# Performance work log

Measured on AMD Instinct MI355X. Metric: run time of the kernel, lower is better.

## Reference

```python
import jax, jax.numpy as jnp
import numpy as np

WINDOW_SIZE = 7
CHANNELS = 3
C1 = 0.01 ** 2
C2 = 0.03 ** 2


def _gaussian_window():
    # 1D gaussian, sigma=1.5, normalized; outer product -> 2D window
    coords = jnp.arange(WINDOW_SIZE, dtype=jnp.float32) - WINDOW_SIZE // 2
    g = jnp.exp(-coords ** 2 / (2 * 1.5 ** 2))
    g = g / g.sum()
    w2d = g[:, None] * g[None, :]  # [7,7]
    # depthwise kernel [C,1,7,7] (OIHW with feature_group_count=C)
    return jnp.tile(w2d[None, None], (CHANNELS, 1, 1, 1))


def _dwconv(x, window):
    pad = WINDOW_SIZE // 2
    return jax.lax.conv_general_dilated(
        x, window,
        window_strides=(1, 1),
        padding=[(pad, pad), (pad, pad)],
        dimension_numbers=('NCHW', 'OIHW', 'NCHW'),
        feature_group_count=CHANNELS,
    )


def setup_inputs() -> dict:
    key = jax.random.key(0)
    k1, k2 = jax.random.split(key)
    shape = (16, 3, 512, 512)
    enhanced = jax.random.uniform(k1, shape, dtype=jnp.float32)
    target = jax.random.uniform(k2, shape, dtype=jnp.float32)
    return {"enhanced": enhanced, "target": target}


def reference(enhanced, target):
    window = _gaussian_window()
    mu1 = _dwconv(enhanced, window)
    mu2 = _dwconv(target, window)
    mu1_sq = mu1 ** 2
    mu2_sq = mu2 ** 2
    mu1_mu2 = mu1 * mu2
    sigma1_sq = _dwconv(enhanced ** 2, window) - mu1_sq
    sigma2_sq = _dwconv(target ** 2, window) - mu2_sq
    sigma12 = _dwconv(enhanced * target, window) - mu1_mu2
    ssim_map = ((2 * mu1_mu2 + C1) * (2 * sigma12 + C2)) / (
        (mu1_sq + mu2_sq + C1) * (sigma1_sq + sigma2_sq + C2))
    return 1.0 - ssim_map.mean()
```

## Files before the change

kernel.cpp:

```cpp
#include <hip/hip_runtime.h>


#define TILE_W 64
#define TILE_H 16
#define HALO 3
#define IN_H 22
#define H_PAIRS 67
#define IMG_H 512
#define IMG_W 512
#define NPLANES 48
#define SSIM_C1 1.0e-4f
#define SSIM_C2 9.0e-4f

static __device__ constexpr float G[7] = {
    0.03663284536f, 0.11128076166f, 0.21674531251f, 0.27068216094f,
    0.21674531251f, 0.11128076166f, 0.03663284536f};

__device__ __forceinline__ float2 pk_fma(const float2 a, const float2 b,
                                         const float2 c) {
  float2 d;
  asm("v_pk_fma_f32 %0, %1, %2, %3" : "=v"(d) : "v"(a), "v"(b), "v"(c));
  return d;
}

__device__ __forceinline__ float4 ld4z(const float* __restrict__ row, int col) {
  if (col >= 0 && col + 3 < IMG_W) {
    return *reinterpret_cast<const float4*>(row + col);
  }
  float4 v;
  v.x = ((unsigned)(col + 0) < IMG_W) ? row[col + 0] : 0.f;
  v.y = ((unsigned)(col + 1) < IMG_W) ? row[col + 1] : 0.f;
  v.z = ((unsigned)(col + 2) < IMG_W) ? row[col + 2] : 0.f;
  v.w = ((unsigned)(col + 3) < IMG_W) ? row[col + 3] : 0.f;
  return v;
}

__global__ __launch_bounds__(256, 6) void ssim_tile_kernel(
    const float* __restrict__ x, const float* __restrict__ y,
    float* __restrict__ partial) {
  __shared__ __align__(16) float2 hbuf[2][IN_H][H_PAIRS];

  const int tid = threadIdx.x;
  const int plane = blockIdx.z;
  const float* __restrict__ xp = x + (size_t)plane * (IMG_H * IMG_W);
  const float* __restrict__ yp = y + (size_t)plane * (IMG_H * IMG_W);
  const int y0 = blockIdx.y * TILE_H - HALO;
  const int x0 = blockIdx.x * TILE_W;
  const bool edge = (blockIdx.x == 0) | (blockIdx.x == gridDim.x - 1) |
                    (blockIdx.y == 0) | (blockIdx.y == gridDim.y - 1);

  if (tid < IN_H * 8) {
    const int hr = tid >> 3;
    const int cg = tid & 7;
    const int bcol = x0 + 8 * cg - 4;
    float wx[16], wy[16];
    const int gy = y0 + hr;
    if (!edge) {
      const float* xr = xp + (size_t)gy * IMG_W + bcol;
      const float* yr = yp + (size_t)gy * IMG_W + bcol;
#pragma unroll
      for (int v = 0; v < 4; ++v) {
        const float4 a = *reinterpret_cast<const float4*>(xr + 4 * v);
        const float4 b = *reinterpret_cast<const float4*>(yr + 4 * v);
        wx[4 * v + 0] = a.x; wx[4 * v + 1] = a.y;
        wx[4 * v + 2] = a.z; wx[4 * v + 3] = a.w;
        wy[4 * v + 0] = b.x; wy[4 * v + 1] = b.y;
        wy[4 * v + 2] = b.z; wy[4 * v + 3] = b.w;
      }
    } else if ((unsigned)gy < IMG_H) {
      const float* xr = xp + (size_t)gy * IMG_W;
      const float* yr = yp + (size_t)gy * IMG_W;
#pragma unroll
      for (int v = 0; v < 4; ++v) {
        const float4 a = ld4z(xr, bcol + 4 * v);
        const float4 b = ld4z(yr, bcol + 4 * v);
        wx[4 * v + 0] = a.x; wx[4 * v + 1] = a.y;
        wx[4 * v + 2] = a.z; wx[4 * v + 3] = a.w;
        wy[4 * v + 0] = b.x; wy[4 * v + 1] = b.y;
        wy[4 * v + 2] = b.z; wy[4 * v + 3] = b.w;
      }
    } else {
#pragma unroll
      for (int i = 0; i < 16; ++i) { wx[i] = 0.f; wy[i] = 0.f; }
    }
    float2 A[8], B[8];
#pragma unroll
    for (int j = 0; j < 8; ++j) {
      A[j] = make_float2(0.f, 0.f);
      B[j] = make_float2(0.f, 0.f);
    }
#pragma unroll
    for (int wi = 1; wi < 15; ++wi) {
      const float xv = wx[wi];
      const float yv = wy[wi];
      const float2 xyp = make_float2(xv, yv);
      const float2 spp = make_float2(fmaf(xv, xv, yv * yv), xv * yv);
#pragma unroll
      for (int j = 0; j < 8; ++j) {
        const int k = wi - 1 - j;
        if (k >= 0 && k < 7) {
          const float2 gk2 = make_float2(G[k], G[k]);
          A[j] = pk_fma(gk2, xyp, A[j]);
          B[j] = pk_fma(gk2, spp, B[j]);
        }
      }
    }
    float2* b0 = &hbuf[0][hr][8 * cg];
    float2* b1 = &hbuf[1][hr][8 * cg];
#pragma unroll
    for (int j = 0; j < 8; ++j) {
      b0[j] = A[j];
      b1[j] = B[j];
    }
  }
  __syncthreads();

  const int c = tid & 63;
  const int r0 = (tid >> 6) * 4;
  float2 M[4], S4[4];
#pragma unroll
  for (int t = 0; t < 4; ++t) {
    M[t] = make_float2(0.f, 0.f);
    S4[t] = make_float2(0.f, 0.f);
  }
#pragma unroll
  for (int j = 0; j < 10; ++j) {
    const float2 mv = hbuf[0][r0 + j][c];
    const float2 sv = hbuf[1][r0 + j][c];
#pragma unroll
    for (int t = 0; t < 4; ++t) {
      const int k = j - t;
      if (k >= 0 && k < 7) {
        const float2 gk2 = make_float2(G[k], G[k]);
        M[t] = pk_fma(gk2, mv, M[t]);
        S4[t] = pk_fma(gk2, sv, S4[t]);
      }
    }
  }

  float acc = 0.f;
#pragma unroll
  for (int t = 0; t < 4; ++t) {
    const float mu1 = M[t].x, mu2 = M[t].y;
    const float eS = S4[t].x, eXY = S4[t].y;
    const float mu12 = mu1 * mu2;
    const float msq = fmaf(mu1, mu1, mu2 * mu2);
    const float sig12 = eXY - mu12;
    const float sigsum = eS - msq;
    const float num = fmaf(2.f, mu12, SSIM_C1) * fmaf(2.f, sig12, SSIM_C2);
    const float den = (msq + SSIM_C1) * (sigsum + SSIM_C2);
    float r = __builtin_amdgcn_rcpf(den);
    r = r * fmaf(-den, r, 2.f);
    acc = fmaf(num, r, acc);
  }

#pragma unroll
  for (int off = 32; off > 0; off >>= 1) acc += __shfl_down(acc, off, 64);
  __shared__ float wsum[4];
  if ((tid & 63) == 0) wsum[tid >> 6] = acc;
  __syncthreads();
  if (tid == 0) {
    const float s = wsum[0] + wsum[1] + wsum[2] + wsum[3];
    partial[(size_t)blockIdx.z * gridDim.x * gridDim.y +
            (size_t)blockIdx.y * gridDim.x + blockIdx.x] = s;
  }
}

__global__ __launch_bounds__(1024) void ssim_reduce_kernel(
    const float* __restrict__ partial, int n, float* __restrict__ out) {
  float acc = 0.f;
  const int nv = n >> 2;
  const float4* __restrict__ p4 = reinterpret_cast<const float4*>(partial);
  for (int i = threadIdx.x; i < nv; i += 1024) {
    const float4 v = p4[i];
    acc += (v.x + v.y) + (v.z + v.w);
  }
#pragma unroll
  for (int off = 32; off > 0; off >>= 1) acc += __shfl_down(acc, off, 64);
  __shared__ float wsum[16];
  if ((threadIdx.x & 63) == 0) wsum[threadIdx.x >> 6] = acc;
  __syncthreads();
  if (threadIdx.x == 0) {
    float s = 0.f;
#pragma unroll
    for (int w = 0; w < 16; ++w) s += wsum[w];
    out[0] = 1.f - s * (1.f / (float)(NPLANES * IMG_H * IMG_W));
  }
}

extern "C" void kernel_launch(void* const* d_in, const int* in_sizes, int n_in,
                              void* d_out, int out_size, void* d_ws, size_t ws_size,
                              hipStream_t stream) {
  const float* enhanced = (const float*)d_in[0];
  const float* target = (const float*)d_in[1];
  float* out = (float*)d_out;
  float* partial = (float*)d_ws;

  dim3 grid(IMG_W / TILE_W, IMG_H / TILE_H, NPLANES);
  dim3 block(256, 1, 1);
  ssim_tile_kernel<<<grid, block, 0, stream>>>(enhanced, target, partial);

  const int nblocks = (IMG_W / TILE_W) * (IMG_H / TILE_H) * NPLANES;
  ssim_reduce_kernel<<<1, 1024, 0, stream>>>(partial, nblocks, out);
}
```

Before: 158.2 us.

## Make each block sweep a full tile row with double-buffered LDS and prefetch

Each block now handles a whole 16-row strip of a plane, looping over the 8 column tiles instead of launching one block per tile. The next tile's global loads are issued before the current tile's vertical pass, and two LDS buffers alternate so that only one barrier per tile is needed. LDS writes are widened to float4, and the row padding changes from 67 to 66 to allow that. The aim is to hide global load latency and cut per-block launch and reduction overhead, at the cost of far fewer blocks (1536), lower occupancy (launch bounds 3) and possible LDS bank conflicts from the new padding.

```diff
diff --git a/kernel.cpp b/kernel.cpp
--- a/kernel.cpp
+++ b/kernel.cpp
@@ -5,10 +5,11 @@
 #define TILE_H 16
 #define HALO 3
 #define IN_H 22
-#define H_PAIRS 67
+#define H_PAIRS 66
 #define IMG_H 512
 #define IMG_W 512
 #define NPLANES 48
+#define NTX 8
 #define SSIM_C1 1.0e-4f
 #define SSIM_C2 9.0e-4f
 
@@ -35,54 +36,68 @@
   return v;
 }
 
-__global__ __launch_bounds__(256, 6) void ssim_tile_kernel(
+__device__ __forceinline__ void lds_barrier() {
+  __builtin_amdgcn_sched_barrier(0);
+  asm volatile("s_waitcnt lgkmcnt(0)" ::: "memory");
+  __builtin_amdgcn_s_barrier();
+  __builtin_amdgcn_sched_barrier(0);
+}
+
+__global__ __launch_bounds__(256, 3) void ssim_row_kernel(
     const float* __restrict__ x, const float* __restrict__ y,
     float* __restrict__ partial) {
-  __shared__ __align__(16) float2 hbuf[2][IN_H][H_PAIRS];
+  __shared__ __align__(16) float2 hbuf[2][2][IN_H][H_PAIRS];
 
   const int tid = threadIdx.x;
-  const int plane = blockIdx.z;
+  const int ty = blockIdx.x;
+  const int plane = blockIdx.y;
   const float* __restrict__ xp = x + (size_t)plane * (IMG_H * IMG_W);
   const float* __restrict__ yp = y + (size_t)plane * (IMG_H * IMG_W);
-  const int y0 = blockIdx.y * TILE_H - HALO;
-  const int x0 = blockIdx.x * TILE_W;
-  const bool edge = (blockIdx.x == 0) | (blockIdx.x == gridDim.x - 1) |
-                    (blockIdx.y == 0) | (blockIdx.y == gridDim.y - 1);
-
-  if (tid < IN_H * 8) {
-    const int hr = tid >> 3;
-    const int cg = tid & 7;
-    const int bcol = x0 + 8 * cg - 4;
-    float wx[16], wy[16];
-    const int gy = y0 + hr;
+  const int y0 = ty * TILE_H - HALO;
+  const bool edge_y = (ty == 0) | (ty == 31);
+
+  const int hr = tid >> 3;
+  const int cg = tid & 7;
+  const bool active = tid < IN_H * 8;
+  const int gy = y0 + hr;
+
+  float4 px[4], py[4];
+
+  auto load_tile = [&](int tx) {
+    const int bcol = tx * TILE_W + 8 * cg - 4;
+    const bool edge = edge_y | (tx == 0) | (tx == NTX - 1);
     if (!edge) {
       const float* xr = xp + (size_t)gy * IMG_W + bcol;
       const float* yr = yp + (size_t)gy * IMG_W + bcol;
 #pragma unroll
       for (int v = 0; v < 4; ++v) {
-        const float4 a = *reinterpret_cast<const float4*>(xr + 4 * v);
-        const float4 b = *reinterpret_cast<const float4*>(yr + 4 * v);
-        wx[4 * v + 0] = a.x; wx[4 * v + 1] = a.y;
-        wx[4 * v + 2] = a.z; wx[4 * v + 3] = a.w;
-        wy[4 * v + 0] = b.x; wy[4 * v + 1] = b.y;
-        wy[4 * v + 2] = b.z; wy[4 * v + 3] = b.w;
+        px[v] = *reinterpret_cast<const float4*>(xr + 4 * v);
+        py[v] = *reinterpret_cast<const float4*>(yr + 4 * v);
       }
     } else if ((unsigned)gy < IMG_H) {
       const float* xr = xp + (size_t)gy * IMG_W;
       const float* yr = yp + (size_t)gy * IMG_W;
 #pragma unroll
       for (int v = 0; v < 4; ++v) {
-        const float4 a = ld4z(xr, bcol + 4 * v);
-        const float4 b = ld4z(yr, bcol + 4 * v);
-        wx[4 * v + 0] = a.x; wx[4 * v + 1] = a.y;
-        wx[4 * v + 2] = a.z; wx[4 * v + 3] = a.w;
-        wy[4 * v + 0] = b.x; wy[4 * v + 1] = b.y;
-        wy[4 * v + 2] = b.z; wy[4 * v + 3] = b.w;
+        px[v] = ld4z(xr, bcol + 4 * v);
+        py[v] = ld4z(yr, bcol + 4 * v);
       }
     } else {
-#pragma unroll
-      for (int i = 0; i < 16; ++i) { wx[i] = 0.f; wy[i] = 0.f; }
-    }
+      const float4 z = make_float4(0.f, 0.f, 0.f, 0.f);
+#pragma unroll
+      for (int v = 0; v < 4; ++v) { px[v] = z; py[v] = z; }
+    }
+  };
+
+  auto h_pass = [&](int b) {
+    const float wx[16] = {px[0].x, px[0].y, px[0].z, px[0].w,
+                          px[1].x, px[1].y, px[1].z, px[1].w,
+                          px[2].x, px[2].y, px[2].z, px[2].w,
+                          px[3].x, px[3].y, px[3].z, px[3].w};
+    const float wy[16] = {py[0].x, py[0].y, py[0].z, py[0].w,
+                          py[1].x, py[1].y, py[1].z, py[1].w,
+                          py[2].x, py[2].y, py[2].z, py[2].w,
+                          py[3].x, py[3].y, py[3].z, py[3].w};
     float2 A[8], B[8];
 #pragma unroll
     for (int j = 0; j < 8; ++j) {
@@ -105,53 +120,66 @@
         }
       }
     }
-    float2* b0 = &hbuf[0][hr][8 * cg];
-    float2* b1 = &hbuf[1][hr][8 * cg];
-#pragma unroll
-    for (int j = 0; j < 8; ++j) {
-      b0[j] = A[j];
-      b1[j] = B[j];
-    }
-  }
-  __syncthreads();
+    float4* w0 = reinterpret_cast<float4*>(&hbuf[b][0][hr][8 * cg]);
+    float4* w1 = reinterpret_cast<float4*>(&hbuf[b][1][hr][8 * cg]);
+#pragma unroll
+    for (int q = 0; q < 4; ++q) {
+      w0[q] = make_float4(A[2 * q].x, A[2 * q].y, A[2 * q + 1].x, A[2 * q + 1].y);
+      w1[q] = make_float4(B[2 * q].x, B[2 * q].y, B[2 * q + 1].x, B[2 * q + 1].y);
+    }
+  };
 
   const int c = tid & 63;
   const int r0 = (tid >> 6) * 4;
-  float2 M[4], S4[4];
-#pragma unroll
-  for (int t = 0; t < 4; ++t) {
-    M[t] = make_float2(0.f, 0.f);
-    S4[t] = make_float2(0.f, 0.f);
-  }
-#pragma unroll
-  for (int j = 0; j < 10; ++j) {
-    const float2 mv = hbuf[0][r0 + j][c];
-    const float2 sv = hbuf[1][r0 + j][c];
+  auto v_pass = [&](int b) -> float {
+    float2 M[4], S4[4];
 #pragma unroll
     for (int t = 0; t < 4; ++t) {
-      const int k = j - t;
-      if (k >= 0 && k < 7) {
-        const float2 gk2 = make_float2(G[k], G[k]);
-        M[t] = pk_fma(gk2, mv, M[t]);
-        S4[t] = pk_fma(gk2, sv, S4[t]);
-      }
-    }
-  }
+      M[t] = make_float2(0.f, 0.f);
+      S4[t] = make_float2(0.f, 0.f);
+    }
+#pragma unroll
+    for (int j = 0; j < 10; ++j) {
+      const float2 mv = hbuf[b][0][r0 + j][c];
+      const float2 sv = hbuf[b][1][r0 + j][c];
+#pragma unroll
+      for (int t = 0; t < 4; ++t) {
+        const int k = j - t;
+        if (k >= 0 && k < 7) {
+          const float2 gk2 = make_float2(G[k], G[k]);
+          M[t] = pk_fma(gk2, mv, M[t]);
+          S4[t] = pk_fma(gk2, sv, S4[t]);
+        }
+      }
+    }
+    float a = 0.f;
+#pragma unroll
+    for (int t = 0; t < 4; ++t) {
+      const float mu1 = M[t].x, mu2 = M[t].y;
+      const float mu12 = mu1 * mu2;
+      const float msq = fmaf(mu1, mu1, mu2 * mu2);
+      const float sig12 = S4[t].y - mu12;
+      const float sigsum = S4[t].x - msq;
+      const float num = fmaf(2.f, mu12, SSIM_C1) * fmaf(2.f, sig12, SSIM_C2);
+      const float den = (msq + SSIM_C1) * (sigsum + SSIM_C2);
+      float r = __builtin_amdgcn_rcpf(den);
+      r = r * fmaf(-den, r, 2.f);
+      a = fmaf(num, r, a);
+    }
+    return a;
+  };
 
   float acc = 0.f;
-#pragma unroll
-  for (int t = 0; t < 4; ++t) {
-    const float mu1 = M[t].x, mu2 = M[t].y;
-    const float eS = S4[t].x, eXY = S4[t].y;
-    const float mu12 = mu1 * mu2;
-    const float msq = fmaf(mu1, mu1, mu2 * mu2);
-    const float sig12 = eXY - mu12;
-    const float sigsum = eS - msq;
-    const float num = fmaf(2.f, mu12, SSIM_C1) * fmaf(2.f, sig12, SSIM_C2);
-    const float den = (msq + SSIM_C1) * (sigsum + SSIM_C2);
-    float r = __builtin_amdgcn_rcpf(den);
-    r = r * fmaf(-den, r, 2.f);
-    acc = fmaf(num, r, acc);
+  if (active) load_tile(0);
+#pragma unroll 2
+  for (int q = 0; q < NTX; ++q) {
+    const int b = q & 1;
+    if (active) {
+      h_pass(b);
+      if (q < NTX - 1) load_tile(q + 1);
+    }
+    lds_barrier();
+    acc += v_pass(b);
   }
 
 #pragma unroll
@@ -160,9 +188,7 @@
   if ((tid & 63) == 0) wsum[tid >> 6] = acc;
   __syncthreads();
   if (tid == 0) {
-    const float s = wsum[0] + wsum[1] + wsum[2] + wsum[3];
-    partial[(size_t)blockIdx.z * gridDim.x * gridDim.y +
-            (size_t)blockIdx.y * gridDim.x + blockIdx.x] = s;
+    partial[(size_t)plane * 32 + ty] = wsum[0] + wsum[1] + wsum[2] + wsum[3];
   }
 }
 
@@ -196,10 +222,10 @@
   float* out = (float*)d_out;
   float* partial = (float*)d_ws;
 
-  dim3 grid(IMG_W / TILE_W, IMG_H / TILE_H, NPLANES);
+  dim3 grid(IMG_H / TILE_H, NPLANES, 1);
   dim3 block(256, 1, 1);
-  ssim_tile_kernel<<<grid, block, 0, stream>>>(enhanced, target, partial);
-
-  const int nblocks = (IMG_W / TILE_W) * (IMG_H / TILE_H) * NPLANES;
+  ssim_row_kernel<<<grid, block, 0, stream>>>(enhanced, target, partial);
+
+  const int nblocks = (IMG_H / TILE_H) * NPLANES;
   ssim_reduce_kernel<<<1, 1024, 0, stream>>>(partial, nblocks, out);
 }
```

After: 145.5 us. 8.0% less time.

## Give each wave its own 16x16 tile to drop block-wide barrier

Applied to the files above, without the earlier changes.

Each block now holds four independent 16x16 tiles, one per wave. Every wave computes its own horizontal pass into a private LDS region and synchronises only with an lgkmcnt wait, so the block-wide __syncthreads between the horizontal and vertical passes is gone. The horizontal results are packed into float4 slots so the vertical pass reads them with one LDS load. The cost is more halo overhead: 22x16 loaded rows per 16x16 tile instead of 22x64 per 64x16 tile, which means roughly double the redundant global reads and horizontal work. Only 44 of 64 lanes are active in the horizontal pass.

```diff
diff --git a/kernel.cpp b/kernel.cpp
--- a/kernel.cpp
+++ b/kernel.cpp
@@ -1,11 +1,10 @@
 #include <hip/hip_runtime.h>
 
 
-#define TILE_W 64
-#define TILE_H 16
+#define MT 16
 #define HALO 3
 #define IN_H 22
-#define H_PAIRS 67
+#define SLOTS 17
 #define IMG_H 512
 #define IMG_W 512
 #define NPLANES 48
@@ -35,54 +34,64 @@
   return v;
 }
 
-__global__ __launch_bounds__(256, 6) void ssim_tile_kernel(
+__global__ __launch_bounds__(256, 4) void ssim_wave_kernel(
     const float* __restrict__ x, const float* __restrict__ y,
     float* __restrict__ partial) {
-  __shared__ __align__(16) float2 hbuf[2][IN_H][H_PAIRS];
+  __shared__ __align__(16) float4 hbuf[4][IN_H][SLOTS];
+  __shared__ float wsum[4];
 
   const int tid = threadIdx.x;
+  const int wid = tid >> 6;
+  const int lane = tid & 63;
+  const int tx = blockIdx.x * 4 + wid;
+  const int ty = blockIdx.y;
   const int plane = blockIdx.z;
   const float* __restrict__ xp = x + (size_t)plane * (IMG_H * IMG_W);
   const float* __restrict__ yp = y + (size_t)plane * (IMG_H * IMG_W);
-  const int y0 = blockIdx.y * TILE_H - HALO;
-  const int x0 = blockIdx.x * TILE_W;
-  const bool edge = (blockIdx.x == 0) | (blockIdx.x == gridDim.x - 1) |
-                    (blockIdx.y == 0) | (blockIdx.y == gridDim.y - 1);
-
-  if (tid < IN_H * 8) {
-    const int hr = tid >> 3;
-    const int cg = tid & 7;
+  const int x0 = tx * MT;
+  const int y0 = ty * MT - HALO;
+  const bool edge = (tx == 0) | (tx == 31) | (ty == 0) | (ty == 31);
+  float4(*mybuf)[SLOTS] = hbuf[wid];
+
+  if (lane < IN_H * 2) {
+    const int r = lane >> 1;
+    const int cg = lane & 1;
+    const int gy = y0 + r;
     const int bcol = x0 + 8 * cg - 4;
-    float wx[16], wy[16];
-    const int gy = y0 + hr;
+    float4 xv0, xv1, xv2, xv3, yv0, yv1, yv2, yv3;
     if (!edge) {
       const float* xr = xp + (size_t)gy * IMG_W + bcol;
       const float* yr = yp + (size_t)gy * IMG_W + bcol;
-#pragma unroll
-      for (int v = 0; v < 4; ++v) {
-        const float4 a = *reinterpret_cast<const float4*>(xr + 4 * v);
-        const float4 b = *reinterpret_cast<const float4*>(yr + 4 * v);
-        wx[4 * v + 0] = a.x; wx[4 * v + 1] = a.y;
-        wx[4 * v + 2] = a.z; wx[4 * v + 3] = a.w;
-        wy[4 * v + 0] = b.x; wy[4 * v + 1] = b.y;
-        wy[4 * v + 2] = b.z; wy[4 * v + 3] = b.w;
-      }
+      xv0 = *reinterpret_cast<const float4*>(xr);
+      xv1 = *reinterpret_cast<const float4*>(xr + 4);
+      xv2 = *reinterpret_cast<const float4*>(xr + 8);
+      xv3 = *reinterpret_cast<const float4*>(xr + 12);
+      yv0 = *reinterpret_cast<const float4*>(yr);
+      yv1 = *reinterpret_cast<const float4*>(yr + 4);
+      yv2 = *reinterpret_cast<const float4*>(yr + 8);
+      yv3 = *reinterpret_cast<const float4*>(yr + 12);
     } else if ((unsigned)gy < IMG_H) {
       const float* xr = xp + (size_t)gy * IMG_W;
       const float* yr = yp + (size_t)gy * IMG_W;
-#pragma unroll
-      for (int v = 0; v < 4; ++v) {
-        const float4 a = ld4z(xr, bcol + 4 * v);
-        const float4 b = ld4z(yr, bcol + 4 * v);
-        wx[4 * v + 0] = a.x; wx[4 * v + 1] = a.y;
-        wx[4 * v + 2] = a.z; wx[4 * v + 3] = a.w;
-        wy[4 * v + 0] = b.x; wy[4 * v + 1] = b.y;
-        wy[4 * v + 2] = b.z; wy[4 * v + 3] = b.w;
-      }
+      xv0 = ld4z(xr, bcol);
+      xv1 = ld4z(xr, bcol + 4);
+      xv2 = ld4z(xr, bcol + 8);
+      xv3 = ld4z(xr, bcol + 12);
+      yv0 = ld4z(yr, bcol);
+      yv1 = ld4z(yr, bcol + 4);
+      yv2 = ld4z(yr, bcol + 8);
+      yv3 = ld4z(yr, bcol + 12);
     } else {
-#pragma unroll
-      for (int i = 0; i < 16; ++i) { wx[i] = 0.f; wy[i] = 0.f; }
-    }
+      const float4 z = make_float4(0.f, 0.f, 0.f, 0.f);
+      xv0 = xv1 = xv2 = xv3 = z;
+      yv0 = yv1 = yv2 = yv3 = z;
+    }
+    const float wx[16] = {xv0.x, xv0.y, xv0.z, xv0.w, xv1.x, xv1.y, xv1.z,
+                          xv1.w, xv2.x, xv2.y, xv2.z, xv2.w, xv3.x, xv3.y,
+                          xv3.z, xv3.w};
+    const float wy[16] = {yv0.x, yv0.y, yv0.z, yv0.w, yv1.x, yv1.y, yv1.z,
+                          yv1.w, yv2.x, yv2.y, yv2.z, yv2.w, yv3.x, yv3.y,
+                          yv3.z, yv3.w};
     float2 A[8], B[8];
 #pragma unroll
     for (int j = 0; j < 8; ++j) {
@@ -105,18 +114,18 @@
         }
       }
     }
-    float2* b0 = &hbuf[0][hr][8 * cg];
-    float2* b1 = &hbuf[1][hr][8 * cg];
 #pragma unroll
     for (int j = 0; j < 8; ++j) {
-      b0[j] = A[j];
-      b1[j] = B[j];
-    }
-  }
-  __syncthreads();
-
-  const int c = tid & 63;
-  const int r0 = (tid >> 6) * 4;
+      mybuf[r][8 * cg + j] = make_float4(A[j].x, A[j].y, B[j].x, B[j].y);
+    }
+  }
+
+  __builtin_amdgcn_sched_barrier(0);
+  asm volatile("s_waitcnt lgkmcnt(0)" ::: "memory");
+  __builtin_amdgcn_sched_barrier(0);
+
+  const int c = lane & 15;
+  const int rg = lane >> 4;
   float2 M[4], S4[4];
 #pragma unroll
   for (int t = 0; t < 4; ++t) {
@@ -125,8 +134,9 @@
   }
 #pragma unroll
   for (int j = 0; j < 10; ++j) {
-    const float2 mv = hbuf[0][r0 + j][c];
-    const float2 sv = hbuf[1][r0 + j][c];
+    const float4 v = mybuf[4 * rg + j][c];
+    const float2 mv = make_float2(v.x, v.y);
+    const float2 sv = make_float2(v.z, v.w);
 #pragma unroll
     for (int t = 0; t < 4; ++t) {
       const int k = j - t;
@@ -137,16 +147,14 @@
       }
     }
   }
-
   float acc = 0.f;
 #pragma unroll
   for (int t = 0; t < 4; ++t) {
     const float mu1 = M[t].x, mu2 = M[t].y;
-    const float eS = S4[t].x, eXY = S4[t].y;
     const float mu12 = mu1 * mu2;
     const float msq = fmaf(mu1, mu1, mu2 * mu2);
-    const float sig12 = eXY - mu12;
-    const float sigsum = eS - msq;
+    const float sig12 = S4[t].y - mu12;
+    const float sigsum = S4[t].x - msq;
     const float num = fmaf(2.f, mu12, SSIM_C1) * fmaf(2.f, sig12, SSIM_C2);
     const float den = (msq + SSIM_C1) * (sigsum + SSIM_C2);
     float r = __builtin_amdgcn_rcpf(den);
@@ -156,13 +164,11 @@
 
 #pragma unroll
   for (int off = 32; off > 0; off >>= 1) acc += __shfl_down(acc, off, 64);
-  __shared__ float wsum[4];
-  if ((tid & 63) == 0) wsum[tid >> 6] = acc;
+  if (lane == 0) wsum[wid] = acc;
   __syncthreads();
   if (tid == 0) {
-    const float s = wsum[0] + wsum[1] + wsum[2] + wsum[3];
-    partial[(size_t)blockIdx.z * gridDim.x * gridDim.y +
-            (size_t)blockIdx.y * gridDim.x + blockIdx.x] = s;
+    partial[((size_t)plane * 32 + ty) * 8 + blockIdx.x] =
+        wsum[0] + wsum[1] + wsum[2] + wsum[3];
   }
 }
 
@@ -196,10 +202,10 @@
   float* out = (float*)d_out;
   float* partial = (float*)d_ws;
 
-  dim3 grid(IMG_W / TILE_W, IMG_H / TILE_H, NPLANES);
+  dim3 grid(8, 32, NPLANES);
   dim3 block(256, 1, 1);
-  ssim_tile_kernel<<<grid, block, 0, stream>>>(enhanced, target, partial);
-
-  const int nblocks = (IMG_W / TILE_W) * (IMG_H / TILE_H) * NPLANES;
+  ssim_wave_kernel<<<grid, block, 0, stream>>>(enhanced, target, partial);
+
+  const int nblocks = 8 * 32 * NPLANES;
   ssim_reduce_kernel<<<1, 1024, 0, stream>>>(partial, nblocks, out);
 }
```

New measurement: 143.8 us. 9.1% less time.
